# Kernel tuning notes

Hardware: AMD Instinct MI355X
Metric: run time of the kernel (lower is better)

Reference implementation:

```python
import jax, jax.numpy as jnp
import numpy as np

N = 100000      # nodes
E = 1600000     # edges (before self-loops)
IN = 256        # in_channels
HID = 16        # num_hid (per-head channels, layer 1)
HEADS = 4
OUT = 16        # out_channels (per-head channels, layer 2)
NEG_SLOPE = 0.2 # PyG GATConv default


def setup_inputs() -> dict:
    key = jax.random.key(0)
    ks = jax.random.split(key, 12)
    def glorot(k, shape, fan):
        return jax.random.normal(k, shape, jnp.float32) * (1.0 / np.sqrt(fan))
    x = jax.random.normal(ks[0], (N, IN), jnp.float32)
    edge_index = jax.random.randint(ks[1], (2, E), 0, N, dtype=jnp.int32)
    W1 = glorot(ks[2], (IN, HEADS * HID), IN)
    att_src1 = glorot(ks[3], (HEADS, HID), HID)
    att_dst1 = glorot(ks[4], (HEADS, HID), HID)
    b1 = jnp.zeros((HEADS * HID,), jnp.float32)
    W2 = glorot(ks[5], (HEADS * HID, HEADS * OUT), HEADS * HID)
    att_src2 = glorot(ks[6], (HEADS, OUT), OUT)
    att_dst2 = glorot(ks[7], (HEADS, OUT), OUT)
    b2 = jnp.zeros((HEADS * OUT,), jnp.float32)
    return {"x": x, "edge_index": edge_index, "W1": W1, "att_src1": att_src1,
            "att_dst1": att_dst1, "b1": b1, "W2": W2, "att_src2": att_src2,
            "att_dst2": att_dst2, "b2": b2}


def gat_conv(x, W, att_src, att_dst, bias, src, dst):
    # PyG GATConv (concat=True): h = xW per head; alpha via segment-softmax over dst.
    H, C = att_src.shape
    n = x.shape[0]
    h = (x @ W).reshape(n, H, C)                    # [N,H,C]
    a_s = jnp.sum(h * att_src, axis=-1)             # [N,H]
    a_d = jnp.sum(h * att_dst, axis=-1)             # [N,H]
    e = jax.nn.leaky_relu(a_s[src] + a_d[dst], NEG_SLOPE)  # [E',H]
    m = jax.lax.stop_gradient(jax.ops.segment_max(e, dst, num_segments=n))
    p = jnp.exp(e - m[dst])
    s = jax.ops.segment_sum(p, dst, num_segments=n)
    alpha = p / (s[dst] + 1e-16)                    # [E',H]
    msg = h[src] * alpha[:, :, None]                # [E',H,C] gathered messages
    out = jax.ops.segment_sum(msg, dst, num_segments=n)
    return out.reshape(n, H * C) + bias


def reference(x, edge_index, W1, att_src1, att_dst1, b1, W2, att_src2, att_dst2, b2):
    # add self loops (PyG GATConv default add_self_loops=True)
    loops = jnp.arange(N, dtype=edge_index.dtype)
    src = jnp.concatenate([edge_index[0], loops])
    dst = jnp.concatenate([edge_index[1], loops])
    h = jax.nn.relu(gat_conv(x, W1, att_src1, att_dst1, b1, src, dst))
    # dropout is identity in eval mode
    return gat_conv(h, W2, att_src2, att_dst2, b2, src, dst)
```

## Files before the change

kernel.cpp:

```cpp
#include <hip/hip_runtime.h>
#include <hip/hip_fp16.h>
#include <cstdint>


#define CH 4096
#define MAXB 512
#define SCAP 6144

using f16x8 = __attribute__((ext_vector_type(8))) _Float16;
using f32x4 = __attribute__((ext_vector_type(4))) float;

__device__ __forceinline__ float lrelu(float v) { return fmaxf(v, 0.2f * v); }

__global__ void ifill_kernel(int* __restrict__ p, int v, int n) {
  int i = blockIdx.x * blockDim.x + threadIdx.x;
  if (i < n) p[i] = v;
}

__global__ void wprep_kernel(const float* __restrict__ W, ushort* __restrict__ WT,
                             int K) {
  int i = blockIdx.x * 256 + threadIdx.x;
  if (i < K * 64) {
    int k = i >> 6, nn = i & 63;
    WT[nn * K + k] = __half_as_ushort(__float2half_rn(W[i]));
  }
}

__global__ __launch_bounds__(256) void bucket_hist(const int* __restrict__ edst,
                                                   int E, int nbuck,
                                                   int* __restrict__ bucket_cnt) {
  __shared__ int hist[MAXB];
  const int t = threadIdx.x;
  for (int j = t; j < MAXB; j += 256) hist[j] = 0;
  __syncthreads();
  const int base = blockIdx.x * CH;
#pragma unroll
  for (int k = 0; k < CH / 256; ++k) {
    int e = base + k * 256 + t;
    if (e < E) atomicAdd(&hist[edst[e] >> 8], 1);
  }
  __syncthreads();
  for (int j = t; j < nbuck; j += 256) {
    int c = hist[j];
    if (c) atomicAdd(&bucket_cnt[j], c);
  }
}

__global__ __launch_bounds__(512) void bucket_scan(const int* __restrict__ bucket_cnt,
                                                   int* __restrict__ bucket_base,
                                                   int* __restrict__ bucket_cursor,
                                                   int nbuck) {
  __shared__ int part[512];
  const int t = threadIdx.x;
  int v = (t < nbuck) ? bucket_cnt[t] : 0;
  part[t] = v;
  __syncthreads();
  for (int off = 1; off < 512; off <<= 1) {
    int u = (t >= off) ? part[t - off] : 0;
    __syncthreads();
    part[t] += u;
    __syncthreads();
  }
  int ex = part[t] - v;
  if (t <= nbuck) {
    int w = (t < nbuck) ? ex : part[nbuck - 1];
    bucket_base[t] = w;
    if (t < nbuck) bucket_cursor[t] = w;
  }
}

__global__ __launch_bounds__(256) void place_kernel(const int* __restrict__ esrc,
                                                    const int* __restrict__ edst,
                                                    int E, int nbuck,
                                                    int* __restrict__ bucket_cursor,
                                                    unsigned int* __restrict__ pairs) {
  __shared__ int hist[MAXB];
  __shared__ int gbase[MAXB];
  __shared__ int rcnt[MAXB];
  const int t = threadIdx.x;
  for (int j = t; j < MAXB; j += 256) { hist[j] = 0; rcnt[j] = 0; }
  __syncthreads();
  const int base = blockIdx.x * CH;
  int b_[CH / 256];
  unsigned int p_[CH / 256];
#pragma unroll
  for (int k = 0; k < CH / 256; ++k) {
    int e = base + k * 256 + t;
    if (e < E) {
      int d = edst[e];
      int s = esrc[e];
      b_[k] = d >> 8;
      p_[k] = ((unsigned int)s << 8) | (unsigned int)(d & 255);
      atomicAdd(&hist[b_[k]], 1);
    } else {
      b_[k] = -1;
    }
  }
  __syncthreads();
  for (int j = t; j < nbuck; j += 256) {
    int c = hist[j];
    gbase[j] = c ? atomicAdd(&bucket_cursor[j], c) : 0;
  }
  __syncthreads();
#pragma unroll
  for (int k = 0; k < CH / 256; ++k) {
    if (b_[k] >= 0) {
      int r = atomicAdd(&rcnt[b_[k]], 1);
      pairs[gbase[b_[k]] + r] = p_[k];
    }
  }
}

__global__ __launch_bounds__(256) void bucket_build(
    const unsigned int* __restrict__ pairs, const int* __restrict__ bucket_base,
    int* __restrict__ ccol, int* __restrict__ start, int* __restrict__ endp,
    int n) {
  __shared__ int cnt[256];
  __shared__ int ls[256];
  __shared__ int csave[256];
  __shared__ int part[256];
  __shared__ int sorted[SCAP];
  const int t = threadIdx.x;
  const int b = blockIdx.x;
  const int d0 = b << 8;
  const int DR = min(256, n - d0);
  const int in_base = bucket_base[b];
  const int nloc = bucket_base[b + 1] - in_base;
  const int out_base = in_base + d0;

  cnt[t] = (t < DR) ? 1 : 0;
  __syncthreads();
  for (int i = t; i < nloc; i += 256)
    atomicAdd(&cnt[pairs[in_base + i] & 255u], 1);
  __syncthreads();
  int c = cnt[t];
  csave[t] = c;
  part[t] = c;
  __syncthreads();
#pragma unroll
  for (int off = 1; off < 256; off <<= 1) {
    int u = (t >= off) ? part[t - off] : 0;
    __syncthreads();
    part[t] += u;
    __syncthreads();
  }
  ls[t] = part[t] - c;
  __syncthreads();
  if (t < DR) {
    int s = out_base + ls[t];
    start[d0 + t] = s;
    endp[d0 + t] = s + csave[t];
    sorted[ls[t]] = d0 + t;
    cnt[t] = 1;
  }
  __syncthreads();
  for (int i = t; i < nloc; i += 256) {
    unsigned int p = pairs[in_base + i];
    int j = (int)(p & 255u);
    int r = atomicAdd(&cnt[j], 1);
    int pos = ls[j] + r;
    if (pos < SCAP) sorted[pos] = (int)(p >> 8);
  }
  __syncthreads();
  int tot = nloc + DR;
  if (tot > SCAP) tot = SCAP;
  for (int i = t; i < tot; i += 256) ccol[out_base + i] = sorted[i];
}

template <int K, bool XHALF>
__global__ __launch_bounds__(256) void gemm_mfma(
    const void* __restrict__ xin, const ushort* __restrict__ wt,
    const float* __restrict__ att_src, const float* __restrict__ att_dst,
    __half* __restrict__ h, float* __restrict__ as_, float* __restrict__ ad_,
    int n) {
  const int tid = threadIdx.x;
  const int w = tid >> 6;
  const int lane = tid & 63;
  const int lr = lane & 15;
  const int kg = lane >> 4;
  const int row0 = blockIdx.x * 64;

  int rr = row0 + w * 16 + lr;
  if (rr > n - 1) rr = n - 1;

  constexpr int NS = K / 32;
  const ushort* wbase = wt + lr * K + kg * 8;

  f16x8 af[NS];
  if constexpr (!XHALF) {
    float4 av[NS][2];
    const float* xp = (const float*)xin + (long long)rr * K + kg * 8;
#pragma unroll
    for (int s = 0; s < NS; ++s) {
      av[s][0] = *(const float4*)(xp + s * 32);
      av[s][1] = *(const float4*)(xp + s * 32 + 4);
    }
#pragma unroll
    for (int s = 0; s < NS; ++s) {
      af[s][0] = (_Float16)av[s][0].x; af[s][1] = (_Float16)av[s][0].y;
      af[s][2] = (_Float16)av[s][0].z; af[s][3] = (_Float16)av[s][0].w;
      af[s][4] = (_Float16)av[s][1].x; af[s][5] = (_Float16)av[s][1].y;
      af[s][6] = (_Float16)av[s][1].z; af[s][7] = (_Float16)av[s][1].w;
    }
  } else {
    const ushort* xp = (const ushort*)xin + (long long)rr * K + kg * 8;
#pragma unroll
    for (int s = 0; s < NS; ++s)
      af[s] = *(const f16x8*)(xp + s * 32);
  }

  f32x4 acc[4] = {};
  f16x8 bcur[4], bnxt[4];
#pragma unroll
  for (int ct = 0; ct < 4; ++ct)
    bcur[ct] = *(const f16x8*)(wbase + ct * 16 * K);
#pragma unroll
  for (int s = 0; s < NS; ++s) {
    if (s + 1 < NS) {
#pragma unroll
      for (int ct = 0; ct < 4; ++ct)
        bnxt[ct] = *(const f16x8*)(wbase + ct * 16 * K + (s + 1) * 32);
    }
#pragma unroll
    for (int ct = 0; ct < 4; ++ct)
      acc[ct] = __builtin_amdgcn_mfma_f32_16x16x32_f16(af[s], bcur[ct], acc[ct], 0, 0, 0);
#pragma unroll
    for (int ct = 0; ct < 4; ++ct) bcur[ct] = bnxt[ct];
  }

  const int wrow = row0 + w * 16 + kg * 4;
#pragma unroll
  for (int ct = 0; ct < 4; ++ct) {
    const float as0 = att_src[ct * 16 + lr];
    const float ad0 = att_dst[ct * 16 + lr];
#pragma unroll
    for (int r = 0; r < 4; ++r) {
      const int row = wrow + r;
      const float v = acc[ct][r];
      if (row < n) h[(long long)row * 64 + ct * 16 + lr] = __float2half_rn(v);
      float s = v * as0, d = v * ad0;
      s += __shfl_xor(s, 1); s += __shfl_xor(s, 2);
      s += __shfl_xor(s, 4); s += __shfl_xor(s, 8);
      d += __shfl_xor(d, 1); d += __shfl_xor(d, 2);
      d += __shfl_xor(d, 4); d += __shfl_xor(d, 8);
      if (lr == 0 && row < n) {
        as_[row * 4 + ct] = s;
        ad_[row * 4 + ct] = d;
      }
    }
  }
}

__global__ __launch_bounds__(256) void node_agg_kernel(
    const int* __restrict__ ccol, const int* __restrict__ start,
    const int* __restrict__ endp,
    const float* __restrict__ as_, const float* __restrict__ ad_,
    const __half2* __restrict__ h2, const float* __restrict__ bias,
    float* __restrict__ fout, __half2* __restrict__ hout, int n, int mode) {
  const int node = blockIdx.x * 8 + (threadIdx.x >> 5);
  if (node >= n) return;
  const int hl = threadIdx.x & 31;
  const int hh = hl >> 3;
  const float adv = ad_[node * 4 + hh];
  const int s0i = start[node];
  const int d = endp[node] - s0i;
  const int* cp = ccol + s0i;
  float ax = 0.f, ay = 0.f, den = 0.f;
  int i = 0;
  for (; i + 4 <= d; i += 4) {
    int s0 = cp[i], s1 = cp[i + 1], s2 = cp[i + 2], s3 = cp[i + 3];
    float p0 = __expf(lrelu(as_[s0 * 4 + hh] + adv));
    float p1 = __expf(lrelu(as_[s1 * 4 + hh] + adv));
    float p2 = __expf(lrelu(as_[s2 * 4 + hh] + adv));
    float p3 = __expf(lrelu(as_[s3 * 4 + hh] + adv));
    float2 h0 = __half22float2(h2[s0 * 32 + hl]);
    float2 h1 = __half22float2(h2[s1 * 32 + hl]);
    float2 h2v = __half22float2(h2[s2 * 32 + hl]);
    float2 h3 = __half22float2(h2[s3 * 32 + hl]);
    den += (p0 + p1) + (p2 + p3);
    ax = fmaf(p0, h0.x, ax); ay = fmaf(p0, h0.y, ay);
    ax = fmaf(p1, h1.x, ax); ay = fmaf(p1, h1.y, ay);
    ax = fmaf(p2, h2v.x, ax); ay = fmaf(p2, h2v.y, ay);
    ax = fmaf(p3, h3.x, ax); ay = fmaf(p3, h3.y, ay);
  }
  for (; i < d; ++i) {
    int s0 = cp[i];
    float p0 = __expf(lrelu(as_[s0 * 4 + hh] + adv));
    float2 h0 = __half22float2(h2[s0 * 32 + hl]);
    den += p0;
    ax = fmaf(p0, h0.x, ax); ay = fmaf(p0, h0.y, ay);
  }
  const float inv = 1.0f / (den + 1e-16f);
  float vx = ax * inv + bias[hl * 2];
  float vy = ay * inv + bias[hl * 2 + 1];
  if (mode == 1) {
    vx = fmaxf(vx, 0.f);
    vy = fmaxf(vy, 0.f);
    hout[node * 32 + hl] = __floats2half2_rn(vx, vy);
  } else {
    *(float2*)(fout + node * 64 + hl * 2) = make_float2(vx, vy);
  }
}

extern "C" void kernel_launch(void* const* d_in, const int* in_sizes, int n_in,
                              void* d_out, int out_size, void* d_ws, size_t ws_size,
                              hipStream_t stream) {
  const float* x = (const float*)d_in[0];
  const int* ei = (const int*)d_in[1];
  const float* W1 = (const float*)d_in[2];
  const float* att_s1 = (const float*)d_in[3];
  const float* att_d1 = (const float*)d_in[4];
  const float* b1 = (const float*)d_in[5];
  const float* W2 = (const float*)d_in[6];
  const float* att_s2 = (const float*)d_in[7];
  const float* att_d2 = (const float*)d_in[8];
  const float* b2 = (const float*)d_in[9];

  const int n = in_sizes[0] / 256;
  const int E = in_sizes[1] / 2;
  const int* esrc = ei;
  const int* edst = ei + E;
  const int nbuck = (n + 255) >> 8;

  float* wsf = (float*)d_ws;
  __half* hbuf = (__half*)wsf;
  float* xbuf = wsf + (long long)n * 64;
  float* as_ = xbuf + (long long)n * 64;
  float* ad_ = as_ + (long long)n * 4;
  int* bucket_cnt = (int*)(ad_ + (long long)n * 4);
  int* bucket_base = bucket_cnt + MAXB;
  int* bucket_cursor = bucket_base + MAXB + 1;
  int* start = bucket_cursor + MAXB;
  int* endp = start + n;
  unsigned int* pairs = (unsigned int*)(endp + n);
  int* ccol = (int*)(pairs + E);
  ushort* wt1 = (ushort*)(((uintptr_t)(ccol + E + n) + 15) & ~(uintptr_t)15);
  ushort* wt2 = wt1 + 64 * 256;
  float* out = (float*)d_out;

  const int ebk = (E + CH - 1) / CH;
  const int gb = (n + 63) / 64;
  const int nb = (n + 7) / 8;

  wprep_kernel<<<(256 * 64 + 255) / 256, 256, 0, stream>>>(W1, wt1, 256);
  wprep_kernel<<<(64 * 64 + 255) / 256, 256, 0, stream>>>(W2, wt2, 64);

  ifill_kernel<<<(MAXB + 255) / 256, 256, 0, stream>>>(bucket_cnt, 0, MAXB);
  bucket_hist<<<ebk, 256, 0, stream>>>(edst, E, nbuck, bucket_cnt);
  bucket_scan<<<1, 512, 0, stream>>>(bucket_cnt, bucket_base, bucket_cursor, nbuck);
  place_kernel<<<ebk, 256, 0, stream>>>(esrc, edst, E, nbuck, bucket_cursor, pairs);
  bucket_build<<<nbuck, 256, 0, stream>>>(pairs, bucket_base, ccol, start, endp, n);

  gemm_mfma<256, false><<<gb, 256, 0, stream>>>(x, wt1, att_s1, att_d1,
                                                hbuf, as_, ad_, n);
  node_agg_kernel<<<nb, 256, 0, stream>>>(ccol, start, endp, as_, ad_,
                                          (const __half2*)hbuf, b1,
                                          nullptr, (__half2*)xbuf, n, 1);

  gemm_mfma<64, true><<<gb, 256, 0, stream>>>(xbuf, wt2, att_s2, att_d2,
                                              hbuf, as_, ad_, n);
  node_agg_kernel<<<nb, 256, 0, stream>>>(ccol, start, endp, as_, ad_,
                                          (const __half2*)hbuf, b2,
                                          out, nullptr, n, 0);
}
```

Before: 232.5 us.

## Fold attention projections into GEMM weights and stage outputs through LDS

Precomputes W·att_src and W·att_dst as eight extra weight columns, padded to a fifth 16-wide MFMA tile, so the attention logits come straight out of the GEMM instead of a per-row shuffle reduction. The GEMM epilogue now stages h and the logits in shared memory and writes them back with coalesced 16-byte stores. This removes the cross-lane shuffles and the scattered 2-byte and 4-byte global stores. In exchange it adds one more MFMA tile per K step, an LDS round trip with a barrier, and fp16 rounding of the folded attention weights.

```diff
diff --git a/kernel.cpp b/kernel.cpp
--- a/kernel.cpp
+++ b/kernel.cpp
@@ -17,13 +17,24 @@
   if (i < n) p[i] = v;
 }
 
-__global__ void wprep_kernel(const float* __restrict__ W, ushort* __restrict__ WT,
-                             int K) {
+__global__ void wprep2_kernel(const float* __restrict__ W,
+                              const float* __restrict__ as,
+                              const float* __restrict__ ad,
+                              ushort* __restrict__ WT, int K) {
   int i = blockIdx.x * 256 + threadIdx.x;
-  if (i < K * 64) {
-    int k = i >> 6, nn = i & 63;
-    WT[nn * K + k] = __half_as_ushort(__float2half_rn(W[i]));
-  }
+  if (i >= 80 * K) return;
+  int c = i / K, k = i % K;
+  float v = 0.f;
+  if (c < 64) {
+    v = W[k * 64 + c];
+  } else if (c < 68) {
+    int hd = c - 64;
+    for (int j = 0; j < 16; ++j) v += W[k * 64 + hd * 16 + j] * as[hd * 16 + j];
+  } else if (c < 72) {
+    int hd = c - 68;
+    for (int j = 0; j < 16; ++j) v += W[k * 64 + hd * 16 + j] * ad[hd * 16 + j];
+  }
+  WT[c * K + k] = __half_as_ushort(__float2half_rn(v));
 }
 
 __global__ __launch_bounds__(256) void bucket_hist(const int* __restrict__ edst,
@@ -170,9 +181,10 @@
 template <int K, bool XHALF>
 __global__ __launch_bounds__(256) void gemm_mfma(
     const void* __restrict__ xin, const ushort* __restrict__ wt,
-    const float* __restrict__ att_src, const float* __restrict__ att_dst,
     __half* __restrict__ h, float* __restrict__ as_, float* __restrict__ ad_,
     int n) {
+  __shared__ _Float16 hs[64 * 88];
+  __shared__ float att[64 * 12];
   const int tid = threadIdx.x;
   const int w = tid >> 6;
   const int lane = tid & 63;
@@ -209,45 +221,44 @@
       af[s] = *(const f16x8*)(xp + s * 32);
   }
 
-  f32x4 acc[4] = {};
-  f16x8 bcur[4], bnxt[4];
+  f32x4 acc[5] = {};
+#pragma unroll
+  for (int s = 0; s < NS; ++s) {
+#pragma unroll
+    for (int ct = 0; ct < 5; ++ct) {
+      f16x8 b = *(const f16x8*)(wbase + ct * 16 * K + s * 32);
+      acc[ct] = __builtin_amdgcn_mfma_f32_16x16x32_f16(af[s], b, acc[ct], 0, 0, 0);
+    }
+  }
+
+  const int orow = w * 16 + kg * 4;
 #pragma unroll
   for (int ct = 0; ct < 4; ++ct)
-    bcur[ct] = *(const f16x8*)(wbase + ct * 16 * K);
-#pragma unroll
-  for (int s = 0; s < NS; ++s) {
-    if (s + 1 < NS) {
-#pragma unroll
-      for (int ct = 0; ct < 4; ++ct)
-        bnxt[ct] = *(const f16x8*)(wbase + ct * 16 * K + (s + 1) * 32);
-    }
-#pragma unroll
-    for (int ct = 0; ct < 4; ++ct)
-      acc[ct] = __builtin_amdgcn_mfma_f32_16x16x32_f16(af[s], bcur[ct], acc[ct], 0, 0, 0);
-#pragma unroll
-    for (int ct = 0; ct < 4; ++ct) bcur[ct] = bnxt[ct];
-  }
-
-  const int wrow = row0 + w * 16 + kg * 4;
-#pragma unroll
-  for (int ct = 0; ct < 4; ++ct) {
-    const float as0 = att_src[ct * 16 + lr];
-    const float ad0 = att_dst[ct * 16 + lr];
-#pragma unroll
-    for (int r = 0; r < 4; ++r) {
-      const int row = wrow + r;
-      const float v = acc[ct][r];
-      if (row < n) h[(long long)row * 64 + ct * 16 + lr] = __float2half_rn(v);
-      float s = v * as0, d = v * ad0;
-      s += __shfl_xor(s, 1); s += __shfl_xor(s, 2);
-      s += __shfl_xor(s, 4); s += __shfl_xor(s, 8);
-      d += __shfl_xor(d, 1); d += __shfl_xor(d, 2);
-      d += __shfl_xor(d, 4); d += __shfl_xor(d, 8);
-      if (lr == 0 && row < n) {
-        as_[row * 4 + ct] = s;
-        ad_[row * 4 + ct] = d;
-      }
-    }
+#pragma unroll
+    for (int r = 0; r < 4; ++r)
+      hs[(orow + r) * 88 + ct * 16 + lr] = (_Float16)acc[ct][r];
+  if (lr < 8) {
+#pragma unroll
+    for (int r = 0; r < 4; ++r)
+      att[(orow + r) * 12 + lr] = acc[4][r];
+  }
+  __syncthreads();
+
+#pragma unroll
+  for (int j = 0; j < 2; ++j) {
+    int s = tid + j * 256;
+    int row = s >> 3, seg = s & 7;
+    if (row0 + row < n)
+      *(uint4*)(h + (long long)(row0 + row) * 64 + seg * 8) =
+          *(const uint4*)&hs[row * 88 + seg * 8];
+  }
+  if (tid < 64) {
+    if (row0 + tid < n)
+      *(float4*)(as_ + (long long)(row0 + tid) * 4) = *(const float4*)&att[tid * 12];
+  } else if (tid < 128) {
+    int t2 = tid - 64;
+    if (row0 + t2 < n)
+      *(float4*)(ad_ + (long long)(row0 + t2) * 4) = *(const float4*)&att[t2 * 12 + 4];
   }
 }
 
@@ -335,15 +346,15 @@
   unsigned int* pairs = (unsigned int*)(endp + n);
   int* ccol = (int*)(pairs + E);
   ushort* wt1 = (ushort*)(((uintptr_t)(ccol + E + n) + 15) & ~(uintptr_t)15);
-  ushort* wt2 = wt1 + 64 * 256;
+  ushort* wt2 = wt1 + 80 * 256;
   float* out = (float*)d_out;
 
   const int ebk = (E + CH - 1) / CH;
   const int gb = (n + 63) / 64;
   const int nb = (n + 7) / 8;
 
-  wprep_kernel<<<(256 * 64 + 255) / 256, 256, 0, stream>>>(W1, wt1, 256);
-  wprep_kernel<<<(64 * 64 + 255) / 256, 256, 0, stream>>>(W2, wt2, 64);
+  wprep2_kernel<<<(80 * 256 + 255) / 256, 256, 0, stream>>>(W1, att_s1, att_d1, wt1, 256);
+  wprep2_kernel<<<(80 * 64 + 255) / 256, 256, 0, stream>>>(W2, att_s2, att_d2, wt2, 64);
 
   ifill_kernel<<<(MAXB + 255) / 256, 256, 0, stream>>>(bucket_cnt, 0, MAXB);
   bucket_hist<<<ebk, 256, 0, stream>>>(edst, E, nbuck, bucket_cnt);
@@ -351,14 +362,12 @@
   place_kernel<<<ebk, 256, 0, stream>>>(esrc, edst, E, nbuck, bucket_cursor, pairs);
   bucket_build<<<nbuck, 256, 0, stream>>>(pairs, bucket_base, ccol, start, endp, n);
 
-  gemm_mfma<256, false><<<gb, 256, 0, stream>>>(x, wt1, att_s1, att_d1,
-                                                hbuf, as_, ad_, n);
+  gemm_mfma<256, false><<<gb, 256, 0, stream>>>(x, wt1, hbuf, as_, ad_, n);
   node_agg_kernel<<<nb, 256, 0, stream>>>(ccol, start, endp, as_, ad_,
                                           (const __half2*)hbuf, b1,
                                           nullptr, (__half2*)xbuf, n, 1);
 
-  gemm_mfma<64, true><<<gb, 256, 0, stream>>>(xbuf, wt2, att_s2, att_d2,
-                                              hbuf, as_, ad_, n);
+  gemm_mfma<64, true><<<gb, 256, 0, stream>>>(xbuf, wt2, hbuf, as_, ad_, n);
   node_agg_kernel<<<nb, 256, 0, stream>>>(ccol, start, endp, as_, ad_,
                                           (const __half2*)hbuf, b2,
                                           out, nullptr, n, 0);
```

Result: faster. 226.8 us (-2.4%).
